# Kernel tuning notes

Measured on AMD Instinct MI355X. Metric: run time of the kernel, lower is better.

The kernel has to match this reference:

```python
import jax, jax.numpy as jnp
import numpy as np

ALPHA = 0.01        # NoiseLayer gaussian scale
P_FEAT = 0.5        # feature dropout (NoiseLayer and TransForm_W)
P_EDGE = 0.4        # graph_corr edge-value dropout
BN_EPS = 1e-5


def setup_inputs() -> dict:
    key = jax.random.key(0)
    k1, k2, k3, k4 = jax.random.split(key, 4)
    N, E, D_IN, D_H = 100000, 1600000, 512, 128
    data = jax.random.normal(k1, (N, D_IN), dtype=jnp.float32)
    adj_indices = jax.random.randint(k2, (2, E), 0, N, dtype=jnp.int64)
    adj_values = jax.random.uniform(k3, (E,), dtype=jnp.float32)
    W = jax.random.normal(k4, (D_IN, D_H), dtype=jnp.float32) * (6.0 / (D_IN + D_H)) ** 0.5
    gamma = jnp.ones((D_H,), dtype=jnp.float32)
    beta = jnp.zeros((D_H,), dtype=jnp.float32)
    return {"data": data, "adj_indices": adj_indices, "adj_values": adj_values,
            "W": W, "gamma": gamma, "beta": beta}


def reference(data, adj_indices, adj_values, W, gamma, beta):
    N = data.shape[0]
    kn, kd1, kd2, ke = jax.random.split(jax.random.key(42), 4)

    # NoiseLayer: x + alpha*randn, then dropout(p=0.5)
    x = data + ALPHA * jax.random.normal(kn, data.shape, data.dtype)
    keep = 1.0 - P_FEAT
    x = x * jax.random.bernoulli(kd1, keep, x.shape).astype(x.dtype) / keep

    # TransForm_W: dropout(p=0.5) then x @ W  -> [N, hidden]
    x = x * jax.random.bernoulli(kd2, keep, x.shape).astype(x.dtype) / keep
    h = x @ W

    # edge-value dropout (graph_corr=0.4) + sparse spmm via segment_sum
    keep_e = 1.0 - P_EDGE
    vals = adj_values * jax.random.bernoulli(ke, keep_e, adj_values.shape).astype(adj_values.dtype) / keep_e
    row, col = adj_indices[0], adj_indices[1]
    msg = vals[:, None] * h[col]                       # [E, hidden]
    agg = jax.ops.segment_sum(msg, row, num_segments=N)  # [N, hidden]

    # ELU activation
    feat = jax.nn.elu(agg)

    # BatchNorm1d (training mode, batch stats over nodes), view_type='spatial'
    mean = feat.mean(axis=0)
    var = feat.var(axis=0)
    feat = gamma * (feat - mean) * jax.lax.rsqrt(var + BN_EPS) + beta
    return feat
```

## Files before the change

### kernel.cpp

```cpp
#include <hip/hip_runtime.h>
#include <stdint.h>

#define N_NODES 100000
#define D_IN 512
#define D_H 128
#define N_EDGES 1600000

__host__ __device__ __forceinline__ void threefry2x32(uint32_t k0, uint32_t k1,
                                                      uint32_t x0, uint32_t x1,
                                                      uint32_t& o0, uint32_t& o1) {
  uint32_t k2 = k0 ^ k1 ^ 0x1BD11BDAu;
  x0 += k0; x1 += k1;
#if defined(__HIP_DEVICE_COMPILE__)
#define ROTL(v, r) __builtin_rotateleft32((v), (r))
#else
#define ROTL(v, r) (((v) << (r)) | ((v) >> (32 - (r))))
#endif
#define TFR(r) x0 += x1; x1 = ROTL(x1, r); x1 ^= x0;
  TFR(13) TFR(15) TFR(26) TFR(6)
  x0 += k1; x1 += k2 + 1u;
  TFR(17) TFR(29) TFR(16) TFR(24)
  x0 += k2; x1 += k0 + 2u;
  TFR(13) TFR(15) TFR(26) TFR(6)
  x0 += k0; x1 += k1 + 3u;
  TFR(17) TFR(29) TFR(16) TFR(24)
  x0 += k1; x1 += k2 + 4u;
  TFR(13) TFR(15) TFR(26) TFR(6)
  x0 += k2; x1 += k0 + 5u;
#undef TFR
#undef ROTL
  o0 = x0; o1 = x1;
}

__device__ __forceinline__ uint32_t tf_bits(uint32_t k0, uint32_t k1, uint32_t i) {
  uint32_t w0, w1;
  threefry2x32(k0, k1, 0u, i, w0, w1);
  return w0 ^ w1;
}

__device__ __forceinline__ float bits_to_unit(uint32_t b) {
  return __uint_as_float((b >> 9) | 0x3f800000u) - 1.0f;
}

__device__ __forceinline__ unsigned short f2bf(float f) {
  uint32_t b = __float_as_uint(f);
  return (unsigned short)((b + 0x7FFFu + ((b >> 16) & 1u)) >> 16);
}

__device__ __forceinline__ float erfinv_fast(float x) {
  float w = -__logf(fmaf(-x, x, 1.0f));
  float wc = w - 2.5f;
  float p = 2.81022636e-08f;
  p = fmaf(p, wc, 3.43273939e-07f);
  p = fmaf(p, wc, -3.5233877e-06f);
  p = fmaf(p, wc, -4.39150654e-06f);
  p = fmaf(p, wc, 0.00021858087f);
  p = fmaf(p, wc, -0.00125372503f);
  p = fmaf(p, wc, -0.00417768164f);
  p = fmaf(p, wc, 0.246640727f);
  p = fmaf(p, wc, 1.50140941f);
  float wt = fmaf(w, rsqrtf(w), -3.0f);
  float q = -0.000200214257f;
  q = fmaf(q, wt, 0.000100950558f);
  q = fmaf(q, wt, 0.00134934322f);
  q = fmaf(q, wt, -0.00367342844f);
  q = fmaf(q, wt, 0.00573950773f);
  q = fmaf(q, wt, -0.0076224613f);
  q = fmaf(q, wt, 0.00943887047f);
  q = fmaf(q, wt, 1.00167406f);
  q = fmaf(q, wt, 2.83297682f);
  return ((w < 5.0f) ? p : q) * x;
}

#define PE 0.60000002384185791f

__global__ __launch_bounds__(256) void prep_kernel(
    const int* __restrict__ adj32, int* __restrict__ flag,
    int* __restrict__ counts, float* __restrict__ stats,
    const float* __restrict__ W, unsigned short* __restrict__ Wt) {
  int idx = blockIdx.x * 256 + threadIdx.x;
  if (blockIdx.x == 0 && threadIdx.x < 64) {
    bool hi_zero = (adj32[2 * threadIdx.x + 1] == 0);
    unsigned long long bl = __ballot(hi_zero);
    if (threadIdx.x == 0) *flag = (bl == ~0ull) ? 1 : 0;
  }
  if (idx < N_NODES) counts[idx] = 0;
  if (idx < 256) stats[idx] = 0.0f;
  if (idx < D_IN * D_H) {
    int k = idx >> 7, n = idx & 127;
    Wt[n * 512 + k] = f2bf(W[idx]);
  }
}

#define GEN_BLKS 25000
#define EDGE_BLKS 6250
#define MAIN_BLKS 31250

__global__ __launch_bounds__(256) void fused_kernel(
    const float* __restrict__ data, unsigned short* __restrict__ x,
    const int* __restrict__ adj32, const int* __restrict__ flag,
    int* __restrict__ counts,
    uint32_t kn0, uint32_t kn1, uint32_t kd10, uint32_t kd11,
    uint32_t kd20, uint32_t kd21, uint32_t ke0, uint32_t ke1) {
  __shared__ uint2 queue[4][512];
  __shared__ unsigned short res[4][512];
  int b = blockIdx.x;
  if ((b % 5) == 4) {
    uint32_t e = (uint32_t)(b / 5) * 256u + threadIdx.x;
    int fl = *flag;
    int r = fl ? adj32[2 * e] : adj32[e];
    uint32_t eb = tf_bits(ke0, ke1, e);
    if (bits_to_unit(eb) < PE) atomicAdd(&counts[r], 1);
    return;
  }
  uint32_t gblk = (uint32_t)(b / 5) * 4u + (uint32_t)(b % 5);
  const int wave = threadIdx.x >> 6, lane = threadIdx.x & 63;
  const uint32_t wbase = gblk * 2048u + (uint32_t)wave * 512u;
  const uint32_t i0 = wbase + (uint32_t)lane * 8u;
  float4 d0 = *(const float4*)(data + i0);
  float4 d1 = *(const float4*)(data + i0 + 4);
  float dv[8] = {d0.x, d0.y, d0.z, d0.w, d1.x, d1.y, d1.z, d1.w};
  *(uint4*)(&res[wave][lane * 8]) = make_uint4(0u, 0u, 0u, 0u);

  uint32_t qc = 0;
#pragma unroll
  for (int j = 0; j < 8; ++j) {
    uint32_t ab = tf_bits(kd10, kd11, i0 + (uint32_t)j);
    bool keep = (ab >> 31) == 0u;
    unsigned long long m = __ballot(keep);
    uint32_t below = __builtin_amdgcn_mbcnt_hi(
        (uint32_t)(m >> 32), __builtin_amdgcn_mbcnt_lo((uint32_t)m, 0u));
    if (keep)
      queue[wave][qc + below] =
          make_uint2(__float_as_uint(dv[j]), (uint32_t)(lane * 8 + j));
    qc += (uint32_t)__popcll(m);
  }

  uint32_t qc2 = 0;
  for (uint32_t k0 = 0; k0 < qc; k0 += 64) {
    uint32_t k = k0 + (uint32_t)lane;
    bool act = k < qc;
    uint2 ent = make_uint2(0u, 0u);
    if (act) ent = queue[wave][k];
    uint32_t bb = tf_bits(kd20, kd21, wbase + ent.y);
    bool keep = act && ((bb >> 31) == 0u);
    unsigned long long m = __ballot(keep);
    uint32_t below = __builtin_amdgcn_mbcnt_hi(
        (uint32_t)(m >> 32), __builtin_amdgcn_mbcnt_lo((uint32_t)m, 0u));
    if (keep) queue[wave][qc2 + below] = ent;
    qc2 += (uint32_t)__popcll(m);
  }

  for (uint32_t k0 = 0; k0 < qc2; k0 += 64) {
    uint32_t k = k0 + (uint32_t)lane;
    bool act = k < qc2;
    uint2 ent = make_uint2(0u, 0u);
    if (act) ent = queue[wave][k];
    uint32_t nb = tf_bits(kn0, kn1, wbase + ent.y);
    float f = bits_to_unit(nb);
    float u = fmaf(f, 2.0f, -0.99999994f);
    float z = erfinv_fast(u);
    float val = fmaf(0.0141421356237f, z, __uint_as_float(ent.x));
    unsigned short r = f2bf(val * 4.0f);
    if (act) res[wave][ent.y] = r;
  }

  uint4 rr = *(const uint4*)(&res[wave][lane * 8]);
  *(uint4*)(x + i0) = rr;
}

typedef __attribute__((ext_vector_type(8))) short bf16x8;
typedef __attribute__((ext_vector_type(4))) float f32x4;
typedef _Float16 half8 __attribute__((ext_vector_type(8)));
#define BM 64
#define BK 64
#define LDT 72

__global__ __launch_bounds__(256) void gemm_kernel(
    const unsigned short* __restrict__ x, const unsigned short* __restrict__ Wt,
    unsigned short* __restrict__ hh) {
  __shared__ __align__(16) unsigned short a_lds[BM * LDT];
  __shared__ __align__(16) unsigned short b_lds[128 * LDT];
  const int tid = threadIdx.x;
  const int r0 = blockIdx.x * BM;
  const int wave = tid >> 6, lane = tid & 63;
  const int lane15 = lane & 15, quad = lane >> 4;
  const int waveM = (wave & 1) * 32, waveN = (wave >> 1) * 64;
  f32x4 acc[2][4] = {};
  for (int kc = 0; kc < D_IN; kc += BK) {
    __syncthreads();
    {
      int row = tid >> 2, q = tid & 3;
      int gr = r0 + row;
      uint4 v0 = make_uint4(0, 0, 0, 0), v1 = v0;
      if (gr < N_NODES) {
        const unsigned short* src = x + (size_t)gr * D_IN + kc + q * 16;
        v0 = *(const uint4*)(src);
        v1 = *(const uint4*)(src + 8);
      }
      *(uint4*)(a_lds + row * LDT + q * 16) = v0;
      *(uint4*)(a_lds + row * LDT + q * 16 + 8) = v1;
    }
    {
      int n = tid >> 1, half = tid & 1;
      const uint4* src = (const uint4*)(Wt + n * 512 + kc + half * 32);
      uint4* dst = (uint4*)(b_lds + n * LDT + half * 32);
      dst[0] = src[0]; dst[1] = src[1]; dst[2] = src[2]; dst[3] = src[3];
    }
    __syncthreads();
    for (int ks = 0; ks < BK; ks += 32) {
      bf16x8 afrag[2], bfrag[4];
      for (int m = 0; m < 2; ++m)
        afrag[m] = *(const bf16x8*)(a_lds + (waveM + m * 16 + lane15) * LDT + ks + quad * 8);
      for (int n = 0; n < 4; ++n)
        bfrag[n] = *(const bf16x8*)(b_lds + (waveN + n * 16 + lane15) * LDT + ks + quad * 8);
      for (int m = 0; m < 2; ++m)
        for (int n = 0; n < 4; ++n)
          acc[m][n] = __builtin_amdgcn_mfma_f32_16x16x32_bf16(afrag[m], bfrag[n], acc[m][n], 0, 0, 0);
    }
  }
  for (int m = 0; m < 2; ++m) {
    int growb = r0 + waveM + m * 16 + quad * 4;
    for (int r = 0; r < 4; ++r) {
      int grow = growb + r;
      if (grow < N_NODES)
        for (int n = 0; n < 4; ++n) {
          _Float16 hv = (_Float16)acc[m][n][r];
          hh[(size_t)grow * D_H + waveN + n * 16 + lane15] =
              __builtin_bit_cast(unsigned short, hv);
        }
    }
  }
}

#define SCAN_B 512
#define SCAN_NBLK ((N_NODES + SCAN_B - 1) / SCAN_B)

__global__ __launch_bounds__(256) void scan1_kernel(const int* __restrict__ counts,
                                                    int* __restrict__ rowstart,
                                                    int* __restrict__ bsums) {
  __shared__ int bufA[SCAN_B], bufB[SCAN_B];
  int t = threadIdx.x, b = blockIdx.x;
  int g0 = b * SCAN_B + t, g1 = g0 + 256;
  int v0 = (g0 < N_NODES) ? counts[g0] : 0;
  int v1 = (g1 < N_NODES) ? counts[g1] : 0;
  bufA[t] = v0; bufA[t + 256] = v1;
  __syncthreads();
  int* src = bufA; int* dst = bufB;
  for (int off = 1; off < SCAN_B; off <<= 1) {
    for (int k = t; k < SCAN_B; k += 256)
      dst[k] = src[k] + ((k >= off) ? src[k - off] : 0);
    __syncthreads();
    int* tmp = src; src = dst; dst = tmp;
  }
  if (g0 < N_NODES) rowstart[g0] = src[t] - v0;
  if (g1 < N_NODES) rowstart[g1] = src[t + 256] - v1;
  if (t == 0) bsums[b] = src[SCAN_B - 1];
}

__global__ __launch_bounds__(256) void scan23_kernel(int* __restrict__ rowstart,
                                                     const int* __restrict__ bsums,
                                                     int* __restrict__ cursor) {
  __shared__ int bufA[256], bufB[256];
  __shared__ int bscan_l[256];
  int t = threadIdx.x;
  int v = (t < SCAN_NBLK) ? bsums[t] : 0;
  bufA[t] = v;
  __syncthreads();
  int* src = bufA; int* dst = bufB;
  for (int off = 1; off < 256; off <<= 1) {
    dst[t] = src[t] + ((t >= off) ? src[t - off] : 0);
    __syncthreads();
    int* tmp = src; src = dst; dst = tmp;
  }
  bscan_l[t] = src[t] - v;
  __syncthreads();
  int i = blockIdx.x * 256 + t;
  if (i < N_NODES) {
    int val = rowstart[i] + bscan_l[i / SCAN_B];
    rowstart[i] = val;
    cursor[i] = val;
  }
}

__global__ __launch_bounds__(256) void scatter_kernel(
    const int* __restrict__ adj32, const int* __restrict__ flag,
    const float* __restrict__ vals, int* __restrict__ cursor,
    int* __restrict__ scol, float* __restrict__ sval,
    uint32_t ke0, uint32_t ke1) {
  uint32_t e = blockIdx.x * 256u + threadIdx.x;
  if (e >= (uint32_t)N_EDGES) return;
  uint32_t eb = tf_bits(ke0, ke1, e);
  if (bits_to_unit(eb) >= PE) return;
  int fl = *flag;
  int r = fl ? adj32[2 * e] : adj32[e];
  int c = fl ? adj32[2 * (N_EDGES + e)] : adj32[N_EDGES + e];
  int pos = atomicAdd(&cursor[r], 1);
  scol[pos] = c;
  sval[pos] = vals[e] / PE;
}

__global__ __launch_bounds__(256) void spmm_csr_kernel(
    const int* __restrict__ scol, const float* __restrict__ sval,
    const int* __restrict__ rowstart, const int* __restrict__ counts,
    const unsigned short* __restrict__ hh, float* __restrict__ agg) {
  int r = blockIdx.x * 4 + (threadIdx.x >> 6);
  if (r >= N_NODES) return;
  int lane = threadIdx.x & 63;
  int g = lane >> 4, l4 = lane & 15;
  int start = rowstart[r], len = counts[r];
  const unsigned short* hp = hh + l4 * 8;
  float acc[8] = {0.f, 0.f, 0.f, 0.f, 0.f, 0.f, 0.f, 0.f};
  int j = 0;
  for (; j + 8 <= len; j += 8) {
    int e0 = start + j + g, e1 = e0 + 4;
    int c0 = scol[e0], c1 = scol[e1];
    float v0 = sval[e0], v1 = sval[e1];
    uint4 b0 = *(const uint4*)(hp + (size_t)c0 * D_H);
    uint4 b1 = *(const uint4*)(hp + (size_t)c1 * D_H);
    half8 x0 = __builtin_bit_cast(half8, b0);
    half8 x1 = __builtin_bit_cast(half8, b1);
#pragma unroll
    for (int k = 0; k < 8; ++k) {
      acc[k] = fmaf(v0, (float)x0[k], acc[k]);
      acc[k] = fmaf(v1, (float)x1[k], acc[k]);
    }
  }
  if (j + g < len) {
    int e = start + j + g;
    int c = scol[e];
    float v = sval[e];
    uint4 bb = *(const uint4*)(hp + (size_t)c * D_H);
    half8 xv = __builtin_bit_cast(half8, bb);
#pragma unroll
    for (int k = 0; k < 8; ++k) acc[k] = fmaf(v, (float)xv[k], acc[k]);
  }
  if (j + 4 + g < len) {
    int e = start + j + 4 + g;
    int c = scol[e];
    float v = sval[e];
    uint4 bb = *(const uint4*)(hp + (size_t)c * D_H);
    half8 xv = __builtin_bit_cast(half8, bb);
#pragma unroll
    for (int k = 0; k < 8; ++k) acc[k] = fmaf(v, (float)xv[k], acc[k]);
  }
#pragma unroll
  for (int k = 0; k < 8; ++k) {
    acc[k] += __shfl_xor(acc[k], 16, 64);
    acc[k] += __shfl_xor(acc[k], 32, 64);
  }
  if (g == 0) {
    float* op = agg + (size_t)r * D_H + l4 * 8;
    *(float4*)op = make_float4(acc[0], acc[1], acc[2], acc[3]);
    *(float4*)(op + 4) = make_float4(acc[4], acc[5], acc[6], acc[7]);
  }
}

__global__ __launch_bounds__(256) void stats_kernel(const float* __restrict__ agg,
                                                    float* __restrict__ stats,
                                                    int rows_per_block) {
  __shared__ float lsum[256], lsq[256];
  int f = threadIdx.x & 127;
  int ro = threadIdx.x >> 7;
  int rstart = blockIdx.x * rows_per_block;
  int rend = min(rstart + rows_per_block, N_NODES);
  float s = 0.f, q = 0.f;
  for (int r = rstart + ro; r < rend; r += 2) {
    float a = agg[(size_t)r * D_H + f];
    float e = a > 0.f ? a : expm1f(a);
    s += e; q += e * e;
  }
  lsum[threadIdx.x] = s; lsq[threadIdx.x] = q;
  __syncthreads();
  if (threadIdx.x < 128) {
    atomicAdd(&stats[f], lsum[threadIdx.x] + lsum[threadIdx.x + 128]);
    atomicAdd(&stats[128 + f], lsq[threadIdx.x] + lsq[threadIdx.x + 128]);
  }
}

__global__ __launch_bounds__(256) void bn_kernel(const float* __restrict__ agg,
                                                 const float* __restrict__ stats,
                                                 const float* __restrict__ gamma,
                                                 const float* __restrict__ beta,
                                                 float* __restrict__ out) {
  int idx4 = blockIdx.x * 256 + threadIdx.x;
  size_t base = (size_t)idx4 * 4;
  if (base >= (size_t)N_NODES * D_H) return;
  int f0 = (int)(base & 127);
  float4 a = *(const float4*)(agg + base);
  float av[4] = {a.x, a.y, a.z, a.w};
  const float inv_n = 1.0f / (float)N_NODES;
  float o[4];
  for (int j = 0; j < 4; ++j) {
    int f = f0 + j;
    float mean = stats[f] * inv_n;
    float var = stats[128 + f] * inv_n - mean * mean;
    float e = av[j] > 0.f ? av[j] : expm1f(av[j]);
    o[j] = gamma[f] * (e - mean) * rsqrtf(var + 1e-5f) + beta[f];
  }
  *(float4*)(out + base) = make_float4(o[0], o[1], o[2], o[3]);
}

extern "C" void kernel_launch(void* const* d_in, const int* in_sizes, int n_in,
                              void* d_out, int out_size, void* d_ws, size_t ws_size,
                              hipStream_t stream) {
  const float* data = (const float*)d_in[0];
  const int* adj = (const int*)d_in[1];
  const float* vals = (const float*)d_in[2];
  const float* W = (const float*)d_in[3];
  const float* gamma = (const float*)d_in[4];
  const float* beta = (const float*)d_in[5];
  float* out = (float*)d_out;

  char* ws = (char*)d_ws;
  unsigned short* x = (unsigned short*)ws;
  float* agg = (float*)ws;
  int* scol = (int*)(ws + 51200000);
  float* sval = (float*)(ws + 57600000);
  int* rowstart = (int*)(ws + 64000000);
  int* cursor = (int*)(ws + 64400000);
  int* bsums = (int*)(ws + 64800000);
  unsigned short* hh = (unsigned short*)(ws + 102400000);
  unsigned short* Wt = (unsigned short*)(ws + 153600000);
  float* stats = (float*)(ws + 153731072);
  int* flag = (int*)(ws + 153732096);
  int* counts = (int*)(ws + 153733120);

  uint32_t kk[4][2];
  for (uint32_t i = 0; i < 4; ++i) threefry2x32(0u, 42u, 0u, i, kk[i][0], kk[i][1]);
  uint32_t kn0 = kk[0][0], kn1 = kk[0][1];
  uint32_t kd10 = kk[1][0], kd11 = kk[1][1];
  uint32_t kd20 = kk[2][0], kd21 = kk[2][1];
  uint32_t ke0 = kk[3][0], ke1 = kk[3][1];

  prep_kernel<<<391, 256, 0, stream>>>(adj, flag, counts, stats, W, Wt);
  fused_kernel<<<MAIN_BLKS, 256, 0, stream>>>(
      data, x, adj, flag, counts,
      kn0, kn1, kd10, kd11, kd20, kd21, ke0, ke1);
  gemm_kernel<<<(N_NODES + BM - 1) / BM, 256, 0, stream>>>(x, Wt, hh);
  scan1_kernel<<<SCAN_NBLK, 256, 0, stream>>>(counts, rowstart, bsums);
  scan23_kernel<<<391, 256, 0, stream>>>(rowstart, bsums, cursor);
  scatter_kernel<<<6250, 256, 0, stream>>>(adj, flag, vals, cursor, scol, sval, ke0, ke1);
  spmm_csr_kernel<<<25000, 256, 0, stream>>>(scol, sval, rowstart, counts, hh, agg);
  stats_kernel<<<1588, 256, 0, stream>>>(agg, stats, 63);
  bn_kernel<<<12500, 256, 0, stream>>>(agg, stats, gamma, beta, out);
}
```

Before: 661.8 us.

## Fuse ELU and BN stats into SpMM, use grid-stride persistent launches

Merges the separate stats pass into the SpMM kernel, which now applies ELU, writes the activated rows and accumulates per-feature sum and sum-of-squares in registers, then reduces them in shared memory and commits them with atomics. This removes one full read of the node-by-hidden aggregate buffer. The BN kernel becomes a single FMA with scale and shift precomputed per thread. The fused, scatter, spmm and bn kernels switch to a fixed 2048-block grid-stride layout to cut block-launch overhead, at the risk of poorer load balance across the irregular rows.

```diff
diff --git a/kernel.cpp b/kernel.cpp
--- a/kernel.cpp
+++ b/kernel.cpp
@@ -73,6 +73,7 @@
 }
 
 #define PE 0.60000002384185791f
+#define GS_BLKS 2048
 
 __global__ __launch_bounds__(256) void prep_kernel(
     const int* __restrict__ adj32, int* __restrict__ flag,
@@ -92,9 +93,7 @@
   }
 }
 
-#define GEN_BLKS 25000
-#define EDGE_BLKS 6250
-#define MAIN_BLKS 31250
+#define MAIN_CHUNKS 31250
 
 __global__ __launch_bounds__(256) void fused_kernel(
     const float* __restrict__ data, unsigned short* __restrict__ x,
@@ -104,69 +103,70 @@
     uint32_t kd20, uint32_t kd21, uint32_t ke0, uint32_t ke1) {
   __shared__ uint2 queue[4][512];
   __shared__ unsigned short res[4][512];
-  int b = blockIdx.x;
-  if ((b % 5) == 4) {
-    uint32_t e = (uint32_t)(b / 5) * 256u + threadIdx.x;
-    int fl = *flag;
-    int r = fl ? adj32[2 * e] : adj32[e];
-    uint32_t eb = tf_bits(ke0, ke1, e);
-    if (bits_to_unit(eb) < PE) atomicAdd(&counts[r], 1);
-    return;
-  }
-  uint32_t gblk = (uint32_t)(b / 5) * 4u + (uint32_t)(b % 5);
   const int wave = threadIdx.x >> 6, lane = threadIdx.x & 63;
-  const uint32_t wbase = gblk * 2048u + (uint32_t)wave * 512u;
-  const uint32_t i0 = wbase + (uint32_t)lane * 8u;
-  float4 d0 = *(const float4*)(data + i0);
-  float4 d1 = *(const float4*)(data + i0 + 4);
-  float dv[8] = {d0.x, d0.y, d0.z, d0.w, d1.x, d1.y, d1.z, d1.w};
-  *(uint4*)(&res[wave][lane * 8]) = make_uint4(0u, 0u, 0u, 0u);
-
-  uint32_t qc = 0;
-#pragma unroll
-  for (int j = 0; j < 8; ++j) {
-    uint32_t ab = tf_bits(kd10, kd11, i0 + (uint32_t)j);
-    bool keep = (ab >> 31) == 0u;
-    unsigned long long m = __ballot(keep);
-    uint32_t below = __builtin_amdgcn_mbcnt_hi(
-        (uint32_t)(m >> 32), __builtin_amdgcn_mbcnt_lo((uint32_t)m, 0u));
-    if (keep)
-      queue[wave][qc + below] =
-          make_uint2(__float_as_uint(dv[j]), (uint32_t)(lane * 8 + j));
-    qc += (uint32_t)__popcll(m);
-  }
-
-  uint32_t qc2 = 0;
-  for (uint32_t k0 = 0; k0 < qc; k0 += 64) {
-    uint32_t k = k0 + (uint32_t)lane;
-    bool act = k < qc;
-    uint2 ent = make_uint2(0u, 0u);
-    if (act) ent = queue[wave][k];
-    uint32_t bb = tf_bits(kd20, kd21, wbase + ent.y);
-    bool keep = act && ((bb >> 31) == 0u);
-    unsigned long long m = __ballot(keep);
-    uint32_t below = __builtin_amdgcn_mbcnt_hi(
-        (uint32_t)(m >> 32), __builtin_amdgcn_mbcnt_lo((uint32_t)m, 0u));
-    if (keep) queue[wave][qc2 + below] = ent;
-    qc2 += (uint32_t)__popcll(m);
-  }
-
-  for (uint32_t k0 = 0; k0 < qc2; k0 += 64) {
-    uint32_t k = k0 + (uint32_t)lane;
-    bool act = k < qc2;
-    uint2 ent = make_uint2(0u, 0u);
-    if (act) ent = queue[wave][k];
-    uint32_t nb = tf_bits(kn0, kn1, wbase + ent.y);
-    float f = bits_to_unit(nb);
-    float u = fmaf(f, 2.0f, -0.99999994f);
-    float z = erfinv_fast(u);
-    float val = fmaf(0.0141421356237f, z, __uint_as_float(ent.x));
-    unsigned short r = f2bf(val * 4.0f);
-    if (act) res[wave][ent.y] = r;
-  }
-
-  uint4 rr = *(const uint4*)(&res[wave][lane * 8]);
-  *(uint4*)(x + i0) = rr;
+  for (uint32_t c = blockIdx.x; c < MAIN_CHUNKS; c += gridDim.x) {
+    if ((c % 5u) == 4u) {
+      uint32_t e = (c / 5u) * 256u + threadIdx.x;
+      int fl = *flag;
+      int r = fl ? adj32[2 * e] : adj32[e];
+      uint32_t eb = tf_bits(ke0, ke1, e);
+      if (bits_to_unit(eb) < PE) atomicAdd(&counts[r], 1);
+      continue;
+    }
+    uint32_t gblk = (c / 5u) * 4u + (c % 5u);
+    const uint32_t wbase = gblk * 2048u + (uint32_t)wave * 512u;
+    const uint32_t i0 = wbase + (uint32_t)lane * 8u;
+    float4 d0 = *(const float4*)(data + i0);
+    float4 d1 = *(const float4*)(data + i0 + 4);
+    float dv[8] = {d0.x, d0.y, d0.z, d0.w, d1.x, d1.y, d1.z, d1.w};
+    *(uint4*)(&res[wave][lane * 8]) = make_uint4(0u, 0u, 0u, 0u);
+
+    uint32_t qc = 0;
+#pragma unroll
+    for (int j = 0; j < 8; ++j) {
+      uint32_t ab = tf_bits(kd10, kd11, i0 + (uint32_t)j);
+      bool keep = (ab >> 31) == 0u;
+      unsigned long long m = __ballot(keep);
+      uint32_t below = __builtin_amdgcn_mbcnt_hi(
+          (uint32_t)(m >> 32), __builtin_amdgcn_mbcnt_lo((uint32_t)m, 0u));
+      if (keep)
+        queue[wave][qc + below] =
+            make_uint2(__float_as_uint(dv[j]), (uint32_t)(lane * 8 + j));
+      qc += (uint32_t)__popcll(m);
+    }
+
+    uint32_t qc2 = 0;
+    for (uint32_t k0 = 0; k0 < qc; k0 += 64) {
+      uint32_t k = k0 + (uint32_t)lane;
+      bool act = k < qc;
+      uint2 ent = make_uint2(0u, 0u);
+      if (act) ent = queue[wave][k];
+      uint32_t bb = tf_bits(kd20, kd21, wbase + ent.y);
+      bool keep = act && ((bb >> 31) == 0u);
+      unsigned long long m = __ballot(keep);
+      uint32_t below = __builtin_amdgcn_mbcnt_hi(
+          (uint32_t)(m >> 32), __builtin_amdgcn_mbcnt_lo((uint32_t)m, 0u));
+      if (keep) queue[wave][qc2 + below] = ent;
+      qc2 += (uint32_t)__popcll(m);
+    }
+
+    for (uint32_t k0 = 0; k0 < qc2; k0 += 64) {
+      uint32_t k = k0 + (uint32_t)lane;
+      bool act = k < qc2;
+      uint2 ent = make_uint2(0u, 0u);
+      if (act) ent = queue[wave][k];
+      uint32_t nb = tf_bits(kn0, kn1, wbase + ent.y);
+      float f = bits_to_unit(nb);
+      float u = fmaf(f, 2.0f, -0.99999994f);
+      float z = erfinv_fast(u);
+      float val = fmaf(0.0141421356237f, z, __uint_as_float(ent.x));
+      unsigned short r = f2bf(val * 4.0f);
+      if (act) res[wave][ent.y] = r;
+    }
+
+    uint4 rr = *(const uint4*)(&res[wave][lane * 8]);
+    *(uint4*)(x + i0) = rr;
+  }
 }
 
 typedef __attribute__((ext_vector_type(8))) short bf16x8;
@@ -288,93 +288,101 @@
     const float* __restrict__ vals, int* __restrict__ cursor,
     int* __restrict__ scol, float* __restrict__ sval,
     uint32_t ke0, uint32_t ke1) {
-  uint32_t e = blockIdx.x * 256u + threadIdx.x;
-  if (e >= (uint32_t)N_EDGES) return;
-  uint32_t eb = tf_bits(ke0, ke1, e);
-  if (bits_to_unit(eb) >= PE) return;
   int fl = *flag;
-  int r = fl ? adj32[2 * e] : adj32[e];
-  int c = fl ? adj32[2 * (N_EDGES + e)] : adj32[N_EDGES + e];
-  int pos = atomicAdd(&cursor[r], 1);
-  scol[pos] = c;
-  sval[pos] = vals[e] / PE;
-}
-
-__global__ __launch_bounds__(256) void spmm_csr_kernel(
+  uint32_t stride = gridDim.x * 256u;
+  for (uint32_t e = blockIdx.x * 256u + threadIdx.x; e < (uint32_t)N_EDGES;
+       e += stride) {
+    uint32_t eb = tf_bits(ke0, ke1, e);
+    if (bits_to_unit(eb) >= PE) continue;
+    int r = fl ? adj32[2 * e] : adj32[e];
+    int c = fl ? adj32[2 * (N_EDGES + e)] : adj32[N_EDGES + e];
+    int pos = atomicAdd(&cursor[r], 1);
+    scol[pos] = c;
+    sval[pos] = vals[e] / PE;
+  }
+}
+
+__global__ __launch_bounds__(256) void spmm_stats_kernel(
     const int* __restrict__ scol, const float* __restrict__ sval,
     const int* __restrict__ rowstart, const int* __restrict__ counts,
-    const unsigned short* __restrict__ hh, float* __restrict__ agg) {
-  int r = blockIdx.x * 4 + (threadIdx.x >> 6);
-  if (r >= N_NODES) return;
-  int lane = threadIdx.x & 63;
-  int g = lane >> 4, l4 = lane & 15;
-  int start = rowstart[r], len = counts[r];
+    const unsigned short* __restrict__ hh, float* __restrict__ agg,
+    float* __restrict__ stats) {
+  __shared__ float ls[4][128], lq[4][128];
+  const int wave = threadIdx.x >> 6, lane = threadIdx.x & 63;
+  const int g = lane >> 4, l4 = lane & 15;
   const unsigned short* hp = hh + l4 * 8;
-  float acc[8] = {0.f, 0.f, 0.f, 0.f, 0.f, 0.f, 0.f, 0.f};
-  int j = 0;
-  for (; j + 8 <= len; j += 8) {
-    int e0 = start + j + g, e1 = e0 + 4;
-    int c0 = scol[e0], c1 = scol[e1];
-    float v0 = sval[e0], v1 = sval[e1];
-    uint4 b0 = *(const uint4*)(hp + (size_t)c0 * D_H);
-    uint4 b1 = *(const uint4*)(hp + (size_t)c1 * D_H);
-    half8 x0 = __builtin_bit_cast(half8, b0);
-    half8 x1 = __builtin_bit_cast(half8, b1);
+  float es[8] = {}, eq[8] = {};
+  const int wstride = gridDim.x * 4;
+  for (int r = blockIdx.x * 4 + wave; r < N_NODES; r += wstride) {
+    int start = rowstart[r], len = counts[r];
+    float acc[8] = {};
+    int j = 0;
+    for (; j + 8 <= len; j += 8) {
+      int e0 = start + j + g, e1 = e0 + 4;
+      int c0 = scol[e0], c1 = scol[e1];
+      float v0 = sval[e0], v1 = sval[e1];
+      uint4 b0 = *(const uint4*)(hp + (size_t)c0 * D_H);
+      uint4 b1 = *(const uint4*)(hp + (size_t)c1 * D_H);
+      half8 x0 = __builtin_bit_cast(half8, b0);
+      half8 x1 = __builtin_bit_cast(half8, b1);
+#pragma unroll
+      for (int k = 0; k < 8; ++k) {
+        acc[k] = fmaf(v0, (float)x0[k], acc[k]);
+        acc[k] = fmaf(v1, (float)x1[k], acc[k]);
+      }
+    }
+    if (j + g < len) {
+      int e = start + j + g;
+      int c = scol[e];
+      float v = sval[e];
+      uint4 bb = *(const uint4*)(hp + (size_t)c * D_H);
+      half8 xv = __builtin_bit_cast(half8, bb);
+#pragma unroll
+      for (int k = 0; k < 8; ++k) acc[k] = fmaf(v, (float)xv[k], acc[k]);
+    }
+    if (j + 4 + g < len) {
+      int e = start + j + 4 + g;
+      int c = scol[e];
+      float v = sval[e];
+      uint4 bb = *(const uint4*)(hp + (size_t)c * D_H);
+      half8 xv = __builtin_bit_cast(half8, bb);
+#pragma unroll
+      for (int k = 0; k < 8; ++k) acc[k] = fmaf(v, (float)xv[k], acc[k]);
+    }
 #pragma unroll
     for (int k = 0; k < 8; ++k) {
-      acc[k] = fmaf(v0, (float)x0[k], acc[k]);
-      acc[k] = fmaf(v1, (float)x1[k], acc[k]);
-    }
-  }
-  if (j + g < len) {
-    int e = start + j + g;
-    int c = scol[e];
-    float v = sval[e];
-    uint4 bb = *(const uint4*)(hp + (size_t)c * D_H);
-    half8 xv = __builtin_bit_cast(half8, bb);
-#pragma unroll
-    for (int k = 0; k < 8; ++k) acc[k] = fmaf(v, (float)xv[k], acc[k]);
-  }
-  if (j + 4 + g < len) {
-    int e = start + j + 4 + g;
-    int c = scol[e];
-    float v = sval[e];
-    uint4 bb = *(const uint4*)(hp + (size_t)c * D_H);
-    half8 xv = __builtin_bit_cast(half8, bb);
-#pragma unroll
-    for (int k = 0; k < 8; ++k) acc[k] = fmaf(v, (float)xv[k], acc[k]);
-  }
-#pragma unroll
-  for (int k = 0; k < 8; ++k) {
-    acc[k] += __shfl_xor(acc[k], 16, 64);
-    acc[k] += __shfl_xor(acc[k], 32, 64);
+      acc[k] += __shfl_xor(acc[k], 16, 64);
+      acc[k] += __shfl_xor(acc[k], 32, 64);
+    }
+    if (g == 0) {
+      float e8[8];
+#pragma unroll
+      for (int k = 0; k < 8; ++k) {
+        float a = acc[k];
+        float e = a > 0.f ? a : expm1f(a);
+        e8[k] = e;
+        es[k] += e;
+        eq[k] += e * e;
+      }
+      float* op = agg + (size_t)r * D_H + l4 * 8;
+      *(float4*)op = make_float4(e8[0], e8[1], e8[2], e8[3]);
+      *(float4*)(op + 4) = make_float4(e8[4], e8[5], e8[6], e8[7]);
+    }
   }
   if (g == 0) {
-    float* op = agg + (size_t)r * D_H + l4 * 8;
-    *(float4*)op = make_float4(acc[0], acc[1], acc[2], acc[3]);
-    *(float4*)(op + 4) = make_float4(acc[4], acc[5], acc[6], acc[7]);
-  }
-}
-
-__global__ __launch_bounds__(256) void stats_kernel(const float* __restrict__ agg,
-                                                    float* __restrict__ stats,
-                                                    int rows_per_block) {
-  __shared__ float lsum[256], lsq[256];
-  int f = threadIdx.x & 127;
-  int ro = threadIdx.x >> 7;
-  int rstart = blockIdx.x * rows_per_block;
-  int rend = min(rstart + rows_per_block, N_NODES);
-  float s = 0.f, q = 0.f;
-  for (int r = rstart + ro; r < rend; r += 2) {
-    float a = agg[(size_t)r * D_H + f];
-    float e = a > 0.f ? a : expm1f(a);
-    s += e; q += e * e;
-  }
-  lsum[threadIdx.x] = s; lsq[threadIdx.x] = q;
+#pragma unroll
+    for (int k = 0; k < 8; ++k) {
+      ls[wave][l4 * 8 + k] = es[k];
+      lq[wave][l4 * 8 + k] = eq[k];
+    }
+  }
   __syncthreads();
   if (threadIdx.x < 128) {
-    atomicAdd(&stats[f], lsum[threadIdx.x] + lsum[threadIdx.x + 128]);
-    atomicAdd(&stats[128 + f], lsq[threadIdx.x] + lsq[threadIdx.x + 128]);
+    int t = threadIdx.x;
+    float s = ls[0][t] + ls[1][t] + ls[2][t] + ls[3][t];
+    float q = lq[0][t] + lq[1][t] + lq[2][t] + lq[3][t];
+    atomicAdd(&stats[t], s);
+    atomicAdd(&stats[128 + t], q);
   }
 }
 
@@ -383,22 +391,31 @@
                                                  const float* __restrict__ gamma,
                                                  const float* __restrict__ beta,
                                                  float* __restrict__ out) {
-  int idx4 = blockIdx.x * 256 + threadIdx.x;
-  size_t base = (size_t)idx4 * 4;
-  if (base >= (size_t)N_NODES * D_H) return;
-  int f0 = (int)(base & 127);
-  float4 a = *(const float4*)(agg + base);
-  float av[4] = {a.x, a.y, a.z, a.w};
   const float inv_n = 1.0f / (float)N_NODES;
-  float o[4];
+  const int tot4 = N_NODES * D_H / 4;
+  int idx0 = blockIdx.x * 256 + threadIdx.x;
+  int stride = gridDim.x * 256;
+  int f0 = (idx0 * 4) & 127;
+  float sc[4], sh[4];
+#pragma unroll
   for (int j = 0; j < 4; ++j) {
     int f = f0 + j;
     float mean = stats[f] * inv_n;
     float var = stats[128 + f] * inv_n - mean * mean;
-    float e = av[j] > 0.f ? av[j] : expm1f(av[j]);
-    o[j] = gamma[f] * (e - mean) * rsqrtf(var + 1e-5f) + beta[f];
-  }
-  *(float4*)(out + base) = make_float4(o[0], o[1], o[2], o[3]);
+    float gsc = gamma[f] * rsqrtf(var + 1e-5f);
+    sc[j] = gsc;
+    sh[j] = beta[f] - mean * gsc;
+  }
+  for (int idx4 = idx0; idx4 < tot4; idx4 += stride) {
+    size_t base = (size_t)idx4 * 4;
+    float4 a = *(const float4*)(agg + base);
+    float4 o;
+    o.x = fmaf(a.x, sc[0], sh[0]);
+    o.y = fmaf(a.y, sc[1], sh[1]);
+    o.z = fmaf(a.z, sc[2], sh[2]);
+    o.w = fmaf(a.w, sc[3], sh[3]);
+    *(float4*)(out + base) = o;
+  }
 }
 
 extern "C" void kernel_launch(void* const* d_in, const int* in_sizes, int n_in,
@@ -434,14 +451,13 @@
   uint32_t ke0 = kk[3][0], ke1 = kk[3][1];
 
   prep_kernel<<<391, 256, 0, stream>>>(adj, flag, counts, stats, W, Wt);
-  fused_kernel<<<MAIN_BLKS, 256, 0, stream>>>(
+  fused_kernel<<<GS_BLKS, 256, 0, stream>>>(
       data, x, adj, flag, counts,
       kn0, kn1, kd10, kd11, kd20, kd21, ke0, ke1);
   gemm_kernel<<<(N_NODES + BM - 1) / BM, 256, 0, stream>>>(x, Wt, hh);
   scan1_kernel<<<SCAN_NBLK, 256, 0, stream>>>(counts, rowstart, bsums);
   scan23_kernel<<<391, 256, 0, stream>>>(rowstart, bsums, cursor);
-  scatter_kernel<<<6250, 256, 0, stream>>>(adj, flag, vals, cursor, scol, sval, ke0, ke1);
-  spmm_csr_kernel<<<25000, 256, 0, stream>>>(scol, sval, rowstart, counts, hh, agg);
-  stats_kernel<<<1588, 256, 0, stream>>>(agg, stats, 63);
-  bn_kernel<<<12500, 256, 0, stream>>>(agg, stats, gamma, beta, out);
-}
+  scatter_kernel<<<GS_BLKS, 256, 0, stream>>>(adj, flag, vals, cursor, scol, sval, ke0, ke1);
+  spmm_stats_kernel<<<GS_BLKS, 256, 0, stream>>>(scol, sval, rowstart, counts, hh, agg, stats);
+  bn_kernel<<<GS_BLKS, 256, 0, stream>>>(agg, stats, gamma, beta, out);
+}
```

Measured after the change: 652.1 us. No clear change (-1.5%).
